# Kernel optimization log

Measured on AMD Instinct MI355X. Metric: run time of the kernel, lower is better.

Reference implementation:

```python
import jax, jax.numpy as jnp
import numpy as np


def setup_inputs() -> dict:
    key = jax.random.key(0)
    k1, k2 = jax.random.split(key)
    B, T, D = 32, 2048, 64
    NUM_CODES = 1024
    z_e = jax.random.normal(k1, (B, T, D), dtype=jnp.float32)
    codebook = jax.random.normal(k2, (NUM_CODES, D), dtype=jnp.float32)
    return {"z_e": z_e, "codebook": codebook}


def reference(z_e, codebook):
    # z_e: [B, T, D], codebook: [K, D]
    B, T, D = z_e.shape
    z_flat = z_e.reshape(-1, D)  # [N, D], N = B*T
    x2 = jnp.sum(z_flat * z_flat, axis=-1, keepdims=True)          # [N, 1]
    c2 = jnp.sum(codebook * codebook, axis=-1)                      # [K]
    xc = jnp.einsum('nd,kd->nk', z_flat, codebook)                  # [N, K]
    dists = x2 - 2.0 * xc + c2[None, :]                              # [N, K]
    indices = jnp.argmin(dists, axis=1)                              # [N]
    z_q = codebook[indices].reshape(B, T, D)
    # Straight-through estimator
    z_q_st = z_e + jax.lax.stop_gradient(z_q - z_e)
    return z_q_st, indices.reshape(B, T)
```

## Files before the change

kernel.cpp:

```cpp
#include <hip/hip_runtime.h>


typedef __attribute__((ext_vector_type(8))) short short8;
typedef __attribute__((ext_vector_type(4))) float f32x4;

#define N_ROWS  65536
#define D       64
#define K_CODES 1024
#define DELTA_H 1.5f
#define CAP     16

#define TILES(F) F(0) F(1) F(2) F(3) F(4) F(5) F(6) F(7)

__device__ __forceinline__ unsigned short f2bf(float f) {
    unsigned u = __builtin_bit_cast(unsigned, f);
    unsigned r = (u + 0x7fffu + ((u >> 16) & 1u)) >> 16;
    return (unsigned short)r;
}

__device__ __forceinline__ short8 cvt8(float4 u, float4 v) {
    short8 r;
    r[0] = (short)f2bf(u.x); r[1] = (short)f2bf(u.y);
    r[2] = (short)f2bf(u.z); r[3] = (short)f2bf(u.w);
    r[4] = (short)f2bf(v.x); r[5] = (short)f2bf(v.y);
    r[6] = (short)f2bf(v.z); r[7] = (short)f2bf(v.w);
    return r;
}

__device__ __forceinline__ float dist_f32(const float* __restrict__ xr,
                                          const float* __restrict__ cr,
                                          float c2k) {
    float a = 0.f, b = 0.f, c = 0.f, d = 0.f;
#pragma unroll
    for (int i = 0; i < 16; i += 2) {
        const float4 x0 = ((const float4*)xr)[i];
        const float4 c0 = ((const float4*)cr)[i];
        const float4 x1 = ((const float4*)xr)[i + 1];
        const float4 c1 = ((const float4*)cr)[i + 1];
        a = fmaf(x0.x, c0.x, a); b = fmaf(x0.y, c0.y, b);
        c = fmaf(x0.z, c0.z, c); d = fmaf(x0.w, c0.w, d);
        a = fmaf(x1.x, c1.x, a); b = fmaf(x1.y, c1.y, b);
        c = fmaf(x1.z, c1.z, c); d = fmaf(x1.w, c1.w, d);
    }
    const float dot = (a + b) + (c + d);
    return fmaf(-2.f, dot, c2k);
}

__global__ __launch_bounds__(256) void prep_kernel(const float* __restrict__ cb,
                                                   float* __restrict__ c2,
                                                   unsigned short* __restrict__ cbb) {
    const int gt = blockIdx.x * 256 + threadIdx.x;
    const int c  = gt >> 2;
    const int q  = gt & 3;
    const float* src = cb + (size_t)c * D + q * 16;
    unsigned short* dst = cbb + (size_t)c * D + q * 16;
    float s = 0.f;
#pragma unroll
    for (int i = 0; i < 2; ++i) {
        const float4 u = ((const float4*)src)[2 * i];
        const float4 v = ((const float4*)src)[2 * i + 1];
        s = fmaf(u.x, u.x, s); s = fmaf(u.y, u.y, s);
        s = fmaf(u.z, u.z, s); s = fmaf(u.w, u.w, s);
        s = fmaf(v.x, v.x, s); s = fmaf(v.y, v.y, s);
        s = fmaf(v.z, v.z, s); s = fmaf(v.w, v.w, s);
        *(short8*)(dst + 8 * i) = cvt8(u, v);
    }
    s += __shfl_xor(s, 1);
    s += __shfl_xor(s, 2);
    if (q == 0) c2[c] = s;
}

__global__ __launch_bounds__(256, 2) void vq_kernel(const float* __restrict__ z_e,
                                                    const float* __restrict__ cb,
                                                    const float* __restrict__ c2g,
                                                    const unsigned short* __restrict__ cbb,
                                                    float* __restrict__ out) {
    __shared__ float qmax_s[4][128];
    __shared__ float gmax_s[128];
    __shared__ int   cnt_s[128];
    __shared__ int   ovf_s[128];
    __shared__ int   win_s[128];
    __shared__ int   cand_s[128][CAP];

    const int tid   = threadIdx.x;
    const int w     = tid >> 6;
    const int lane  = tid & 63;
    const int lcol  = lane & 15;
    const int lk    = lane >> 4;
    const int rbase = blockIdx.x * 128;

    if (tid < 128) { cnt_s[tid] = 0; ovf_s[tid] = 0; }

#define DECLA(i) short8 a0_##i, a1_##i;
    TILES(DECLA)
#define LOADA(i)                                                               \
    {                                                                          \
        const float* p = z_e + (size_t)(rbase + 16 * (i) + lcol) * D + 8 * lk; \
        a0_##i = cvt8(*(const float4*)p,        *(const float4*)(p + 4));      \
        a1_##i = cvt8(*(const float4*)(p + 32), *(const float4*)(p + 36));     \
    }
    TILES(LOADA)

    const unsigned short* bp  = cbb + (size_t)(w * 256 + lcol) * D + 8 * lk;
    const float*          c2p = c2g + w * 256 + lcol;

#define LOADB(T)                                                      \
    bn0 = *(const short8*)(bp + (size_t)(T) * 1024);                  \
    bn1 = *(const short8*)(bp + (size_t)(T) * 1024 + 32);             \
    c2n = c2p[(T) * 16];

#define MFMA16()                                                               \
    const float sv = -0.5f * c2c;                                              \
    _Pragma("unroll")                                                          \
    TILES(DOMFMA)

#define DOMFMA(i)                                                              \
    f32x4 acc##i = {sv, sv, sv, sv};                                           \
    acc##i = __builtin_amdgcn_mfma_f32_16x16x32_bf16(a0_##i, bc0, acc##i, 0, 0, 0); \
    acc##i = __builtin_amdgcn_mfma_f32_16x16x32_bf16(a1_##i, bc1, acc##i, 0, 0, 0);

#define DECLM(i) float m##i##0 = -3.4e38f, m##i##1 = -3.4e38f,                 \
                       m##i##2 = -3.4e38f, m##i##3 = -3.4e38f;
    TILES(DECLM)
    {
        short8 bc0, bc1, bn0, bn1;
        float c2c, c2n;
        LOADB(0);
        bc0 = bn0; bc1 = bn1; c2c = c2n;
        for (int tt = 0; tt < 16; ++tt) {
            if (tt < 15) { LOADB(tt + 1); }
            {
                const float sv = -0.5f * c2c;
#define DOTILE1(i)                                                                    \
                f32x4 acc##i = {sv, sv, sv, sv};                                      \
                acc##i = __builtin_amdgcn_mfma_f32_16x16x32_bf16(a0_##i, bc0, acc##i, 0, 0, 0); \
                acc##i = __builtin_amdgcn_mfma_f32_16x16x32_bf16(a1_##i, bc1, acc##i, 0, 0, 0); \
                m##i##0 = fmaxf(m##i##0, acc##i[0]);                                  \
                m##i##1 = fmaxf(m##i##1, acc##i[1]);                                  \
                m##i##2 = fmaxf(m##i##2, acc##i[2]);                                  \
                m##i##3 = fmaxf(m##i##3, acc##i[3]);
                TILES(DOTILE1)
            }
            bc0 = bn0; bc1 = bn1; c2c = c2n;
        }
    }

#define REDT(i)                                                       \
    m##i##0 = fmaxf(m##i##0, __shfl_xor(m##i##0, OFF));               \
    m##i##1 = fmaxf(m##i##1, __shfl_xor(m##i##1, OFF));               \
    m##i##2 = fmaxf(m##i##2, __shfl_xor(m##i##2, OFF));               \
    m##i##3 = fmaxf(m##i##3, __shfl_xor(m##i##3, OFF));
    {
#define OFF 1
        TILES(REDT)
#undef OFF
#define OFF 2
        TILES(REDT)
#undef OFF
#define OFF 4
        TILES(REDT)
#undef OFF
#define OFF 8
        TILES(REDT)
#undef OFF
    }

    if (lcol == 0) {
#define WRQ(i)                                                        \
        qmax_s[w][16 * (i) + 4 * lk + 0] = m##i##0;                   \
        qmax_s[w][16 * (i) + 4 * lk + 1] = m##i##1;                   \
        qmax_s[w][16 * (i) + 4 * lk + 2] = m##i##2;                   \
        qmax_s[w][16 * (i) + 4 * lk + 3] = m##i##3;
        TILES(WRQ)
    }
    __syncthreads();
    if (tid < 128) {
        gmax_s[tid] = fmaxf(fmaxf(qmax_s[0][tid], qmax_s[1][tid]),
                            fmaxf(qmax_s[2][tid], qmax_s[3][tid]));
    }
    __syncthreads();

#define DECLH(i)                                                      \
    const float h##i##0 = gmax_s[16 * (i) + 4 * lk + 0] - DELTA_H;    \
    const float h##i##1 = gmax_s[16 * (i) + 4 * lk + 1] - DELTA_H;    \
    const float h##i##2 = gmax_s[16 * (i) + 4 * lk + 2] - DELTA_H;    \
    const float h##i##3 = gmax_s[16 * (i) + 4 * lk + 3] - DELTA_H;
    TILES(DECLH)
#define MIN4(i) fminf(fminf(h##i##0, h##i##1), fminf(h##i##2, h##i##3))
    const float gmin = fminf(
        fminf(fminf(MIN4(0), MIN4(1)), fminf(MIN4(2), MIN4(3))),
        fminf(fminf(MIN4(4), MIN4(5)), fminf(MIN4(6), MIN4(7))));

#define REC(RL, CODE)                                                 \
    {                                                                 \
        const int sl = atomicAdd(&cnt_s[RL], 1);                      \
        if (sl < CAP) cand_s[RL][sl] = (CODE); else ovf_s[RL] = 1;    \
    }

    {
        short8 bc0, bc1, bn0, bn1;
        float c2c, c2n;
        LOADB(0);
        bc0 = bn0; bc1 = bn1; c2c = c2n;
        for (int tt = 0; tt < 16; ++tt) {
            if (tt < 15) { LOADB(tt + 1); }
            {
                const float sv = -0.5f * c2c;
#define DOTILE2(i)                                                                    \
                f32x4 acc##i = {sv, sv, sv, sv};                                      \
                acc##i = __builtin_amdgcn_mfma_f32_16x16x32_bf16(a0_##i, bc0, acc##i, 0, 0, 0); \
                acc##i = __builtin_amdgcn_mfma_f32_16x16x32_bf16(a1_##i, bc1, acc##i, 0, 0, 0);
                TILES(DOTILE2)
#define MAX4(i) fmaxf(fmaxf(acc##i[0], acc##i[1]), fmaxf(acc##i[2], acc##i[3]))
                const float tm = fmaxf(
                    fmaxf(fmaxf(MAX4(0), MAX4(1)), fmaxf(MAX4(2), MAX4(3))),
                    fmaxf(fmaxf(MAX4(4), MAX4(5)), fmaxf(MAX4(6), MAX4(7))));
                if (tm >= gmin) {
                    const int code = (w << 8) + (tt << 4) + lcol;
#define CHK(i)                                                            \
                    if (acc##i[0] >= h##i##0) REC(16 * (i) + 4 * lk + 0, code); \
                    if (acc##i[1] >= h##i##1) REC(16 * (i) + 4 * lk + 1, code); \
                    if (acc##i[2] >= h##i##2) REC(16 * (i) + 4 * lk + 2, code); \
                    if (acc##i[3] >= h##i##3) REC(16 * (i) + 4 * lk + 3, code);
                    TILES(CHK)
                }
            }
            bc0 = bn0; bc1 = bn1; c2c = c2n;
        }
    }
    __syncthreads();

    if (tid < 128) {
        const int grow = rbase + tid;
        const int cnt  = cnt_s[tid];
        int win;
        if (ovf_s[tid] == 0 && cnt == 1) {
            win = cand_s[tid][0];
        } else {
            const float* xr = z_e + (size_t)grow * D;
            float bestd = 3.4e38f;
            int   bi    = K_CODES;
            if (ovf_s[tid]) {
                for (int k = 0; k < K_CODES; ++k) {
                    const float dk = dist_f32(xr, cb + (size_t)k * D, c2g[k]);
                    if (dk < bestd || (dk == bestd && k < bi)) { bestd = dk; bi = k; }
                }
            } else {
                for (int j = 0; j < cnt; ++j) {
                    const int k = cand_s[tid][j];
                    const float dk = dist_f32(xr, cb + (size_t)k * D, c2g[k]);
                    if (dk < bestd || (dk == bestd && k < bi)) { bestd = dk; bi = k; }
                }
            }
            win = bi;
        }
        win_s[tid] = win;
        out[(size_t)N_ROWS * D + grow] = (float)win;
    }
    __syncthreads();

    {
        const int rl   = tid >> 1;
        const int hf   = tid & 1;
        const int grow = rbase + rl;
        const float4* src = (const float4*)(cb + (size_t)win_s[rl] * D) + hf * 8;
        float4*       dst = (float4*)(out + (size_t)grow * D) + hf * 8;
#pragma unroll
        for (int i = 0; i < 8; ++i) dst[i] = src[i];
    }
}

extern "C" void kernel_launch(void* const* d_in, const int* in_sizes, int n_in,
                              void* d_out, int out_size, void* d_ws, size_t ws_size,
                              hipStream_t stream) {
    const float* z_e = (const float*)d_in[0];
    const float* cb  = (const float*)d_in[1];
    float* out = (float*)d_out;
    float*          c2  = (float*)d_ws;
    unsigned short* cbb = (unsigned short*)((char*)d_ws + 4096);

    hipLaunchKernelGGL(prep_kernel, dim3(16), dim3(256), 0, stream, cb, c2, cbb);
    hipLaunchKernelGGL(vq_kernel, dim3(N_ROWS / 128), dim3(256), 0, stream,
                       z_e, cb, c2, cbb, out);
}
```

Before: 119.0 us.

## Split codebook across 12 waves per block and stage z_e tile in LDS

Raises the block from 4 to 12 waves, giving each wave an uneven slice of the 64 code tiles (5 or 6) in place of a fixed 16-tile quarter. The z_e tile is converted to bf16 once into padded shared memory and read by all waves, rather than each wave loading and converting it from global memory. The aim is more waves in flight per CU to hide latency across the two MFMA passes. In exchange it adds LDS use, a larger cross-wave max reduction and an extra barrier, and the 8 tiles of A operands per wave may hold occupancy down through register pressure.

```diff
diff --git a/kernel.cpp b/kernel.cpp
--- a/kernel.cpp
+++ b/kernel.cpp
@@ -9,6 +9,8 @@
 #define K_CODES 1024
 #define DELTA_H 1.5f
 #define CAP     16
+#define WAVES   12
+#define ZSTRIDE 72
 
 #define TILES(F) F(0) F(1) F(2) F(3) F(4) F(5) F(6) F(7)
 
@@ -70,12 +72,13 @@
     if (q == 0) c2[c] = s;
 }
 
-__global__ __launch_bounds__(256, 2) void vq_kernel(const float* __restrict__ z_e,
+__global__ __launch_bounds__(768, 3) void vq_kernel(const float* __restrict__ z_e,
                                                     const float* __restrict__ cb,
                                                     const float* __restrict__ c2g,
                                                     const unsigned short* __restrict__ cbb,
                                                     float* __restrict__ out) {
-    __shared__ float qmax_s[4][128];
+    __shared__ unsigned short zA[128 * ZSTRIDE];
+    __shared__ float qmax_s[WAVES][128];
     __shared__ float gmax_s[128];
     __shared__ int   cnt_s[128];
     __shared__ int   ovf_s[128];
@@ -91,33 +94,36 @@
 
     if (tid < 128) { cnt_s[tid] = 0; ovf_s[tid] = 0; }
 
+    if (tid < 512) {
+        const int row = tid >> 2;
+        const int q   = tid & 3;
+        const float4* src = (const float4*)(z_e + (size_t)(rbase + row) * D + q * 16);
+        unsigned short* dst = zA + row * ZSTRIDE + q * 16;
+        *(short8*)(dst)     = cvt8(src[0], src[1]);
+        *(short8*)(dst + 8) = cvt8(src[2], src[3]);
+    }
+    __syncthreads();
+
 #define DECLA(i) short8 a0_##i, a1_##i;
     TILES(DECLA)
 #define LOADA(i)                                                               \
     {                                                                          \
-        const float* p = z_e + (size_t)(rbase + 16 * (i) + lcol) * D + 8 * lk; \
-        a0_##i = cvt8(*(const float4*)p,        *(const float4*)(p + 4));      \
-        a1_##i = cvt8(*(const float4*)(p + 32), *(const float4*)(p + 36));     \
+        const unsigned short* p = zA + (16 * (i) + lcol) * ZSTRIDE + 8 * lk;   \
+        a0_##i = *(const short8*)(p);                                          \
+        a1_##i = *(const short8*)(p + 32);                                     \
     }
     TILES(LOADA)
 
-    const unsigned short* bp  = cbb + (size_t)(w * 256 + lcol) * D + 8 * lk;
-    const float*          c2p = c2g + w * 256 + lcol;
+    const int sw = (16 * w) / 3;
+    const int ew = (16 * (w + 1)) / 3;
+
+    const unsigned short* bp  = cbb + (size_t)lcol * D + 8 * lk;
+    const float*          c2p = c2g + lcol;
 
 #define LOADB(T)                                                      \
     bn0 = *(const short8*)(bp + (size_t)(T) * 1024);                  \
     bn1 = *(const short8*)(bp + (size_t)(T) * 1024 + 32);             \
     c2n = c2p[(T) * 16];
-
-#define MFMA16()                                                               \
-    const float sv = -0.5f * c2c;                                              \
-    _Pragma("unroll")                                                          \
-    TILES(DOMFMA)
-
-#define DOMFMA(i)                                                              \
-    f32x4 acc##i = {sv, sv, sv, sv};                                           \
-    acc##i = __builtin_amdgcn_mfma_f32_16x16x32_bf16(a0_##i, bc0, acc##i, 0, 0, 0); \
-    acc##i = __builtin_amdgcn_mfma_f32_16x16x32_bf16(a1_##i, bc1, acc##i, 0, 0, 0);
 
 #define DECLM(i) float m##i##0 = -3.4e38f, m##i##1 = -3.4e38f,                 \
                        m##i##2 = -3.4e38f, m##i##3 = -3.4e38f;
@@ -125,10 +131,10 @@
     {
         short8 bc0, bc1, bn0, bn1;
         float c2c, c2n;
-        LOADB(0);
+        LOADB(sw);
         bc0 = bn0; bc1 = bn1; c2c = c2n;
-        for (int tt = 0; tt < 16; ++tt) {
-            if (tt < 15) { LOADB(tt + 1); }
+        for (int tt = sw; tt < ew; ++tt) {
+            { const int tn = (tt + 1 < 64) ? tt + 1 : 63; LOADB(tn); }
             {
                 const float sv = -0.5f * c2c;
 #define DOTILE1(i)                                                                    \
@@ -175,8 +181,10 @@
     }
     __syncthreads();
     if (tid < 128) {
-        gmax_s[tid] = fmaxf(fmaxf(qmax_s[0][tid], qmax_s[1][tid]),
-                            fmaxf(qmax_s[2][tid], qmax_s[3][tid]));
+        float g = qmax_s[0][tid];
+#pragma unroll
+        for (int ww = 1; ww < WAVES; ++ww) g = fmaxf(g, qmax_s[ww][tid]);
+        gmax_s[tid] = g;
     }
     __syncthreads();
 
@@ -200,10 +208,10 @@
     {
         short8 bc0, bc1, bn0, bn1;
         float c2c, c2n;
-        LOADB(0);
+        LOADB(sw);
         bc0 = bn0; bc1 = bn1; c2c = c2n;
-        for (int tt = 0; tt < 16; ++tt) {
-            if (tt < 15) { LOADB(tt + 1); }
+        for (int tt = sw; tt < ew; ++tt) {
+            { const int tn = (tt + 1 < 64) ? tt + 1 : 63; LOADB(tn); }
             {
                 const float sv = -0.5f * c2c;
 #define DOTILE2(i)                                                                    \
@@ -216,7 +224,7 @@
                     fmaxf(fmaxf(MAX4(0), MAX4(1)), fmaxf(MAX4(2), MAX4(3))),
                     fmaxf(fmaxf(MAX4(4), MAX4(5)), fmaxf(MAX4(6), MAX4(7))));
                 if (tm >= gmin) {
-                    const int code = (w << 8) + (tt << 4) + lcol;
+                    const int code = (tt << 4) + lcol;
 #define CHK(i)                                                            \
                     if (acc##i[0] >= h##i##0) REC(16 * (i) + 4 * lk + 0, code); \
                     if (acc##i[1] >= h##i##1) REC(16 * (i) + 4 * lk + 1, code); \
@@ -259,14 +267,14 @@
     }
     __syncthreads();
 
-    {
-        const int rl   = tid >> 1;
-        const int hf   = tid & 1;
+    if (tid < 512) {
+        const int rl   = tid >> 2;
+        const int q    = tid & 3;
         const int grow = rbase + rl;
-        const float4* src = (const float4*)(cb + (size_t)win_s[rl] * D) + hf * 8;
-        float4*       dst = (float4*)(out + (size_t)grow * D) + hf * 8;
-#pragma unroll
-        for (int i = 0; i < 8; ++i) dst[i] = src[i];
+        const float4* src = (const float4*)(cb + (size_t)win_s[rl] * D) + q * 4;
+        float4*       dst = (float4*)(out + (size_t)grow * D) + q * 4;
+#pragma unroll
+        for (int i = 0; i < 4; ++i) dst[i] = src[i];
     }
 }
 
@@ -280,6 +288,6 @@
     unsigned short* cbb = (unsigned short*)((char*)d_ws + 4096);
 
     hipLaunchKernelGGL(prep_kernel, dim3(16), dim3(256), 0, stream, cb, c2, cbb);
-    hipLaunchKernelGGL(vq_kernel, dim3(N_ROWS / 128), dim3(256), 0, stream,
+    hipLaunchKernelGGL(vq_kernel, dim3(N_ROWS / 128), dim3(768), 0, stream,
                        z_e, cb, c2, cbb, out);
 }
```

After: 121.2 us. About the same (+1.8%).
